# Performance work log

Hardware: AMD Instinct MI355X
Metric: run time of the kernel (lower is better)

The kernel has to match this reference:

```python
import jax, jax.numpy as jnp
import numpy as np
from jax.scipy.special import logsumexp

ITERS = 50
EPS = 0.005
B, N, D = 8, 2048, 3


def _sq_cost(x, y):
    x2 = jnp.sum(x * x, axis=-1)  # [B,N]
    y2 = jnp.sum(y * y, axis=-1)  # [B,M]
    c = x2[:, :, None] + y2[:, None, :] - 2.0 * jnp.einsum('bnd,bmd->bnm', x, y)
    return jnp.maximum(c, 0.0)


def setup_inputs() -> dict:
    key = jax.random.key(0)
    k1, k2 = jax.random.split(key)
    input1 = jax.random.normal(k1, (B, N, D), dtype=jnp.float32)
    input2 = jax.random.normal(k2, (B, N, D), dtype=jnp.float32)
    return {"input1": input1, "input2": input2}


def reference(input1, input2):
    # Approximate EMD between equal-size point sets, as in emdModule(x, y, eps, iters):
    # iterative entropic-regularized (Sinkhorn/auction-style) assignment on the
    # squared-distance cost, eps = entropic temperature, iters = sweeps.
    eps = jnp.float32(EPS)
    b, n, _ = input1.shape
    m = input2.shape[1]
    C = _sq_cost(input1, input2)  # [B,N,M]
    log_mu = -jnp.log(jnp.float32(n))
    log_nu = -jnp.log(jnp.float32(m))

    def body(carry, _):
        f, g = carry  # duals [B,N], [B,M]
        f = eps * (log_mu - logsumexp((g[:, None, :] - C) / eps, axis=2))
        g = eps * (log_nu - logsumexp((f[:, :, None] - C) / eps, axis=1))
        return (f, g), None

    f0 = jnp.zeros((b, n), dtype=C.dtype)
    g0 = jnp.zeros((b, m), dtype=C.dtype)
    (f, g), _ = jax.lax.scan(body, (f0, g0), None, length=ITERS)

    # transport plan; each row sums to 1/N (soft assignment)
    P = jnp.exp((f[:, :, None] + g[:, None, :] - C) / eps)  # [B,N,M]
    # per-point assigned squared distance (dis of emdModule), then .mean()
    dis = jnp.sum(P * C, axis=-1) * jnp.float32(n)  # [B,N]
    return jnp.mean(dis)
```

## Files before the change

kernel.cpp:

```cpp
#include <hip/hip_runtime.h>
#include <math.h>

#define NB 8
#define NN 2048
#define NM 2048
#define NITERS 50

static constexpr float F_EPS  = 0.005f;
static constexpr float LOG2E  = 1.4426950408889634f;
static constexpr float KK     = LOG2E / F_EPS;
static constexpr float TWOK   = 2.0f * KK;
static constexpr float NEG_LOG2N = -11.0f;

__device__ __forceinline__ float fexp2(float x) { return __builtin_amdgcn_exp2f(x); }
__device__ __forceinline__ float flog2(float x) { return __builtin_amdgcn_logf(x); }

__global__ void pack_init(const float* __restrict__ V, float4* __restrict__ Pout, int total)
{
    int i = blockIdx.x * blockDim.x + threadIdx.x;
    if (i < total) {
        float v0 = V[3*i], v1 = V[3*i+1], v2 = V[3*i+2];
        float s  = fmaf(v0, v0, fmaf(v1, v1, v2*v2));
        Pout[i]  = make_float4(v0, v1, v2, -KK * s);
    }
}

__global__ __launch_bounds__(256, 4) void sink_update(
    const float4* __restrict__ Pin,
    const float*  __restrict__ Vraw,
    float4*       __restrict__ Pout)
{
    __shared__ float2 part [32][65];
    __shared__ float2 part2[32][9];
    const int tid  = threadIdx.x;
    const int lane = tid & 63;
    const int wave = tid >> 6;
    const int wgs_per_b = NN / 32;
    const int b       = blockIdx.x / wgs_per_b;
    const int rowbase = (blockIdx.x % wgs_per_b) * 32;

    float xs0[8], xs1[8], xs2[8];
    {
        const float* vb = Vraw + ((size_t)(b * NN + rowbase + wave * 8)) * 3;
        #pragma unroll
        for (int r = 0; r < 8; ++r) {
            xs0[r] = TWOK * vb[r*3+0];
            xs1[r] = TWOK * vb[r*3+1];
            xs2[r] = TWOK * vb[r*3+2];
        }
    }

    const float4* __restrict__ pp = Pin + b * NM + lane;

    float rm[8], rs[8];
    #pragma unroll
    for (int r = 0; r < 8; ++r) { rm[r] = -1e30f; rs[r] = 0.f; }

    for (int ib = 0; ib < 8; ++ib) {
        const float4 p0 = pp[(ib*4 + 0) * 64];
        const float4 p1 = pp[(ib*4 + 1) * 64];
        const float4 p2 = pp[(ib*4 + 2) * 64];
        const float4 p3 = pp[(ib*4 + 3) * 64];
        #pragma unroll
        for (int r = 0; r < 8; ++r) {
            const float z0 = fmaf(xs0[r], p0.x, fmaf(xs1[r], p0.y, fmaf(xs2[r], p0.z, p0.w)));
            const float z1 = fmaf(xs0[r], p1.x, fmaf(xs1[r], p1.y, fmaf(xs2[r], p1.z, p1.w)));
            const float z2 = fmaf(xs0[r], p2.x, fmaf(xs1[r], p2.y, fmaf(xs2[r], p2.z, p2.w)));
            const float z3 = fmaf(xs0[r], p3.x, fmaf(xs1[r], p3.y, fmaf(xs2[r], p3.z, p3.w)));
            const float cm = fmaxf(fmaxf(z0, z1), fmaxf(z2, z3));
            const float nm = fmaxf(rm[r], cm);
            const float s  = (fexp2(z0 - nm) + fexp2(z1 - nm))
                           + (fexp2(z2 - nm) + fexp2(z3 - nm));
            rs[r] = fmaf(rs[r], fexp2(rm[r] - nm), s);
            rm[r] = nm;
        }
    }

    #pragma unroll
    for (int r = 0; r < 8; ++r) part[wave*8 + r][lane] = make_float2(rm[r], rs[r]);
    __syncthreads();

    {
        const int row = tid >> 3, seg = tid & 7;
        float m8 = -1e30f;
        float2 v[8];
        #pragma unroll
        for (int k = 0; k < 8; ++k) { v[k] = part[row][seg*8 + k]; m8 = fmaxf(m8, v[k].x); }
        float s8 = 0.f;
        #pragma unroll
        for (int k = 0; k < 8; ++k) s8 = fmaf(v[k].y, fexp2(v[k].x - m8), s8);
        part2[row][seg] = make_float2(m8, s8);
    }
    __syncthreads();

    if (tid < 32) {
        float gm = -1e30f;
        float2 v[8];
        #pragma unroll
        for (int k = 0; k < 8; ++k) { v[k] = part2[tid][k]; gm = fmaxf(gm, v[k].x); }
        float s = 0.f;
        #pragma unroll
        for (int k = 0; k < 8; ++k) s = fmaf(v[k].y, fexp2(v[k].x - gm), s);
        const float lse2 = gm + flog2(s);
        const int n0 = rowbase + tid;
        const float* vp = Vraw + ((size_t)(b * NN + n0)) * 3;
        Pout[b * NN + n0] = make_float4(vp[0], vp[1], vp[2], NEG_LOG2N - lse2);
    }
}

__global__ __launch_bounds__(256, 4) void final_loss(
    const float4* __restrict__ Px, const float4* __restrict__ Py,
    float* __restrict__ out)
{
    __shared__ float wsum[4];
    const int tid  = threadIdx.x;
    const int lane = tid & 63;
    const int wave = tid >> 6;
    const int wgs_per_b = NN / 32;
    const int b       = blockIdx.x / wgs_per_b;
    const int rowbase = (blockIdx.x % wgs_per_b) * 32;

    float xr0[8], xr1[8], xr2[8], Af[8], xq[8];
    {
        const float4* xb = Px + b * NN + rowbase + wave * 8;
        #pragma unroll
        for (int r = 0; r < 8; ++r) {
            const float4 xp = xb[r];
            xr0[r] = xp.x; xr1[r] = xp.y; xr2[r] = xp.z; Af[r] = xp.w;
            xq[r]  = fmaf(xp.x, xp.x, fmaf(xp.y, xp.y, xp.z * xp.z));
        }
    }

    const float4* __restrict__ pp = Py + b * NM + lane;

    float acc = 0.f;
    for (int i = 0; i < 32; ++i) {
        const float4 p = pp[i * 64];
        const float ysq = fmaf(p.x, p.x, fmaf(p.y, p.y, p.z * p.z));
        #pragma unroll
        for (int r = 0; r < 8; ++r) {
            const float dot = fmaf(xr0[r], p.x, fmaf(xr1[r], p.y, xr2[r] * p.z));
            const float cc  = fmaxf(fmaf(-2.f, dot, xq[r] + ysq), 0.f);
            const float zp  = fmaf(TWOK, dot, Af[r] + p.w);
            acc = fmaf(fexp2(zp), cc, acc);
        }
    }
    #pragma unroll
    for (int o = 32; o > 0; o >>= 1) acc += __shfl_xor(acc, o);
    if (lane == 0) wsum[wave] = acc;
    __syncthreads();
    if (tid == 0) {
        atomicAdd(out, (wsum[0] + wsum[1] + wsum[2] + wsum[3]) * (1.0f / NB));
    }
}

extern "C" void kernel_launch(void* const* d_in, const int* in_sizes, int n_in,
                              void* d_out, int out_size, void* d_ws, size_t ws_size,
                              hipStream_t stream)
{
    const float* x = (const float*)d_in[0];
    const float* y = (const float*)d_in[1];
    float4* Px = (float4*)d_ws;
    float4* Py = Px + NB * NN;

    pack_init<<<(NB * NM + 255) / 256, 256, 0, stream>>>(y, Py, NB * NM);

    for (int it = 0; it < NITERS; ++it) {
        sink_update<<<NB * NN / 32, 256, 0, stream>>>(Py, x, Px);
        sink_update<<<NB * NM / 32, 256, 0, stream>>>(Px, y, Py);
    }

    hipMemsetAsync(d_out, 0, sizeof(float), stream);
    final_loss<<<NB * NN / 32, 256, 0, stream>>>(Px, Py, (float*)d_out);
}
```

Measured before the change: 1.147 ms.

## Fuse all Sinkhorn sweeps into one persistent kernel with per-batch grid barriers

Replaces the 100 sink_update launches plus the init and final-loss kernels with a single persistent kernel of 512 workgroups. Each group of 64 workgroups, one per batch, synchronises through an atomic counter barrier with sleep-polling between half-sweeps. This removes per-launch overhead and the gaps between dependent kernels. In exchange it depends on all 512 workgroups being co-resident, since otherwise the spin barrier deadlocks, and it adds atomic polling cost at every phase.

After: 3.504 ms. +205.3%, slower.

```diff
diff --git a/kernel.cpp b/kernel.cpp
--- a/kernel.cpp
+++ b/kernel.cpp
@@ -15,33 +15,37 @@
 __device__ __forceinline__ float fexp2(float x) { return __builtin_amdgcn_exp2f(x); }
 __device__ __forceinline__ float flog2(float x) { return __builtin_amdgcn_logf(x); }
 
-__global__ void pack_init(const float* __restrict__ V, float4* __restrict__ Pout, int total)
-{
-    int i = blockIdx.x * blockDim.x + threadIdx.x;
-    if (i < total) {
-        float v0 = V[3*i], v1 = V[3*i+1], v2 = V[3*i+2];
-        float s  = fmaf(v0, v0, fmaf(v1, v1, v2*v2));
-        Pout[i]  = make_float4(v0, v1, v2, -KK * s);
-    }
-}
-
-__global__ __launch_bounds__(256, 4) void sink_update(
-    const float4* __restrict__ Pin,
-    const float*  __restrict__ Vraw,
-    float4*       __restrict__ Pout)
-{
-    __shared__ float2 part [32][65];
-    __shared__ float2 part2[32][9];
+struct SmemT {
+    float2 part [32][65];
+    float2 part2[32][9];
+    float  wsum[4];
+};
+
+__device__ __forceinline__ void batch_barrier(int* cnt, int phase)
+{
+    __syncthreads();
+    if (threadIdx.x == 0) {
+        __hip_atomic_fetch_add(cnt, 1, __ATOMIC_RELEASE, __HIP_MEMORY_SCOPE_AGENT);
+        const int target = 64 * phase;
+        while (__hip_atomic_load(cnt, __ATOMIC_ACQUIRE, __HIP_MEMORY_SCOPE_AGENT) < target)
+            __builtin_amdgcn_s_sleep(1);
+    }
+    __syncthreads();
+}
+
+__device__ __forceinline__ void half_sweep(
+    const float4* __restrict__ Pin_b,
+    const float*  __restrict__ Vrow,
+    float4*       __restrict__ Pout_row,
+    SmemT& sm)
+{
     const int tid  = threadIdx.x;
     const int lane = tid & 63;
     const int wave = tid >> 6;
-    const int wgs_per_b = NN / 32;
-    const int b       = blockIdx.x / wgs_per_b;
-    const int rowbase = (blockIdx.x % wgs_per_b) * 32;
 
     float xs0[8], xs1[8], xs2[8];
     {
-        const float* vb = Vraw + ((size_t)(b * NN + rowbase + wave * 8)) * 3;
+        const float* vb = Vrow + (size_t)(wave * 8) * 3;
         #pragma unroll
         for (int r = 0; r < 8; ++r) {
             xs0[r] = TWOK * vb[r*3+0];
@@ -50,7 +54,7 @@
         }
     }
 
-    const float4* __restrict__ pp = Pin + b * NM + lane;
+    const float4* __restrict__ pp = Pin_b + lane;
 
     float rm[8], rs[8];
     #pragma unroll
@@ -77,7 +81,7 @@
     }
 
     #pragma unroll
-    for (int r = 0; r < 8; ++r) part[wave*8 + r][lane] = make_float2(rm[r], rs[r]);
+    for (int r = 0; r < 8; ++r) sm.part[wave*8 + r][lane] = make_float2(rm[r], rs[r]);
     __syncthreads();
 
     {
@@ -85,11 +89,11 @@
         float m8 = -1e30f;
         float2 v[8];
         #pragma unroll
-        for (int k = 0; k < 8; ++k) { v[k] = part[row][seg*8 + k]; m8 = fmaxf(m8, v[k].x); }
+        for (int k = 0; k < 8; ++k) { v[k] = sm.part[row][seg*8 + k]; m8 = fmaxf(m8, v[k].x); }
         float s8 = 0.f;
         #pragma unroll
         for (int k = 0; k < 8; ++k) s8 = fmaf(v[k].y, fexp2(v[k].x - m8), s8);
-        part2[row][seg] = make_float2(m8, s8);
+        sm.part2[row][seg] = make_float2(m8, s8);
     }
     __syncthreads();
 
@@ -97,60 +101,86 @@
         float gm = -1e30f;
         float2 v[8];
         #pragma unroll
-        for (int k = 0; k < 8; ++k) { v[k] = part2[tid][k]; gm = fmaxf(gm, v[k].x); }
+        for (int k = 0; k < 8; ++k) { v[k] = sm.part2[tid][k]; gm = fmaxf(gm, v[k].x); }
         float s = 0.f;
         #pragma unroll
         for (int k = 0; k < 8; ++k) s = fmaf(v[k].y, fexp2(v[k].x - gm), s);
         const float lse2 = gm + flog2(s);
-        const int n0 = rowbase + tid;
-        const float* vp = Vraw + ((size_t)(b * NN + n0)) * 3;
-        Pout[b * NN + n0] = make_float4(vp[0], vp[1], vp[2], NEG_LOG2N - lse2);
-    }
-}
-
-__global__ __launch_bounds__(256, 4) void final_loss(
-    const float4* __restrict__ Px, const float4* __restrict__ Py,
-    float* __restrict__ out)
-{
-    __shared__ float wsum[4];
-    const int tid  = threadIdx.x;
-    const int lane = tid & 63;
-    const int wave = tid >> 6;
-    const int wgs_per_b = NN / 32;
-    const int b       = blockIdx.x / wgs_per_b;
-    const int rowbase = (blockIdx.x % wgs_per_b) * 32;
-
-    float xr0[8], xr1[8], xr2[8], Af[8], xq[8];
+        const float* vp = Vrow + (size_t)tid * 3;
+        Pout_row[tid] = make_float4(vp[0], vp[1], vp[2], NEG_LOG2N - lse2);
+    }
+    __syncthreads();
+}
+
+__global__ __launch_bounds__(256, 2) void sinkhorn_persist(
+    const float* __restrict__ X, const float* __restrict__ Y,
+    float4* __restrict__ Px, float4* __restrict__ Py,
+    int* __restrict__ cnt, float* __restrict__ out)
+{
+    __shared__ SmemT sm;
+    const int tid     = threadIdx.x;
+    const int b       = blockIdx.x & 7;
+    const int rowbase = (blockIdx.x >> 3) * 32;
+    int* mycnt = cnt + b * 16;
+
+    const float*  Xrow = X + ((size_t)(b * NN + rowbase)) * 3;
+    const float*  Yrow = Y + ((size_t)(b * NM + rowbase)) * 3;
+    float4* PxRow = Px + b * NN + rowbase;
+    float4* PyRow = Py + b * NM + rowbase;
+    const float4* PxB = Px + b * NN;
+    const float4* PyB = Py + b * NM;
+
+    if (tid < 32) {
+        const float* vp = Yrow + (size_t)tid * 3;
+        const float v0 = vp[0], v1 = vp[1], v2 = vp[2];
+        const float sq = fmaf(v0, v0, fmaf(v1, v1, v2*v2));
+        PyRow[tid] = make_float4(v0, v1, v2, -KK * sq);
+    }
+
+    int phase = 1;
+    batch_barrier(mycnt, phase);
+
+    #pragma unroll 1
+    for (int it = 0; it < NITERS; ++it) {
+        half_sweep(PyB, Xrow, PxRow, sm);
+        batch_barrier(mycnt, ++phase);
+        half_sweep(PxB, Yrow, PyRow, sm);
+        batch_barrier(mycnt, ++phase);
+    }
+
     {
-        const float4* xb = Px + b * NN + rowbase + wave * 8;
+        const int lane = tid & 63;
+        const int wave = tid >> 6;
+
+        float xr0[8], xr1[8], xr2[8], Af[8], xq[8];
+        const float4* xb = PxRow + wave * 8;
         #pragma unroll
         for (int r = 0; r < 8; ++r) {
             const float4 xp = xb[r];
             xr0[r] = xp.x; xr1[r] = xp.y; xr2[r] = xp.z; Af[r] = xp.w;
             xq[r]  = fmaf(xp.x, xp.x, fmaf(xp.y, xp.y, xp.z * xp.z));
         }
-    }
-
-    const float4* __restrict__ pp = Py + b * NM + lane;
-
-    float acc = 0.f;
-    for (int i = 0; i < 32; ++i) {
-        const float4 p = pp[i * 64];
-        const float ysq = fmaf(p.x, p.x, fmaf(p.y, p.y, p.z * p.z));
-        #pragma unroll
-        for (int r = 0; r < 8; ++r) {
-            const float dot = fmaf(xr0[r], p.x, fmaf(xr1[r], p.y, xr2[r] * p.z));
-            const float cc  = fmaxf(fmaf(-2.f, dot, xq[r] + ysq), 0.f);
-            const float zp  = fmaf(TWOK, dot, Af[r] + p.w);
-            acc = fmaf(fexp2(zp), cc, acc);
-        }
-    }
-    #pragma unroll
-    for (int o = 32; o > 0; o >>= 1) acc += __shfl_xor(acc, o);
-    if (lane == 0) wsum[wave] = acc;
-    __syncthreads();
-    if (tid == 0) {
-        atomicAdd(out, (wsum[0] + wsum[1] + wsum[2] + wsum[3]) * (1.0f / NB));
+
+        const float4* __restrict__ pp = PyB + lane;
+        float acc = 0.f;
+        for (int i = 0; i < 32; ++i) {
+            const float4 p = pp[i * 64];
+            const float ysq = fmaf(p.x, p.x, fmaf(p.y, p.y, p.z * p.z));
+            #pragma unroll
+            for (int r = 0; r < 8; ++r) {
+                const float dot = fmaf(xr0[r], p.x, fmaf(xr1[r], p.y, xr2[r] * p.z));
+                const float cc  = fmaxf(fmaf(-2.f, dot, xq[r] + ysq), 0.f);
+                const float zp  = fmaf(TWOK, dot, Af[r] + p.w);
+                acc = fmaf(fexp2(zp), cc, acc);
+            }
+        }
+        #pragma unroll
+        for (int o = 32; o > 0; o >>= 1) acc += __shfl_xor(acc, o);
+        if (lane == 0) sm.wsum[wave] = acc;
+        __syncthreads();
+        if (tid == 0) {
+            atomicAdd(out, (sm.wsum[0] + sm.wsum[1] + sm.wsum[2] + sm.wsum[3]) * (1.0f / NB));
+        }
     }
 }
 
@@ -162,14 +192,10 @@
     const float* y = (const float*)d_in[1];
     float4* Px = (float4*)d_ws;
     float4* Py = Px + NB * NN;
-
-    pack_init<<<(NB * NM + 255) / 256, 256, 0, stream>>>(y, Py, NB * NM);
-
-    for (int it = 0; it < NITERS; ++it) {
-        sink_update<<<NB * NN / 32, 256, 0, stream>>>(Py, x, Px);
-        sink_update<<<NB * NM / 32, 256, 0, stream>>>(Px, y, Py);
-    }
-
+    int*    cnt = (int*)((char*)d_ws + (size_t)(NB * NN + NB * NM) * sizeof(float4));
+
+    hipMemsetAsync(cnt, 0, NB * 16 * sizeof(int), stream);
     hipMemsetAsync(d_out, 0, sizeof(float), stream);
-    final_loss<<<NB * NN / 32, 256, 0, stream>>>(Px, Py, (float*)d_out);
-}
+
+    sinkhorn_persist<<<NB * NN / 32, 256, 0, stream>>>(x, y, Px, Py, cnt, (float*)d_out);
+}
```

## Split column range across waves and double-buffer column loads

Applied to the files above, without the earlier changes.

Each workgroup now covers 16 rows instead of 32. Its four waves are arranged as 2 row-groups by 2 column halves, so each wave scans 1024 columns instead of all 2048. This doubles the grid to 1024 blocks for better occupancy across the CUs. The column-point loads are software-prefetched one batch ahead so global latency overlaps the exp/FMA work. In exchange the shared-memory reduction becomes wider (16 partials per row), and each column point is read by twice as many workgroups.

Result: faster. 1.120 ms (-2.4%).

```diff
diff --git a/kernel.cpp b/kernel.cpp
--- a/kernel.cpp
+++ b/kernel.cpp
@@ -30,18 +30,20 @@
     const float*  __restrict__ Vraw,
     float4*       __restrict__ Pout)
 {
-    __shared__ float2 part [32][65];
-    __shared__ float2 part2[32][9];
+    __shared__ float2 part [16][129];
+    __shared__ float2 part2[16][17];
     const int tid  = threadIdx.x;
     const int lane = tid & 63;
     const int wave = tid >> 6;
-    const int wgs_per_b = NN / 32;
+    const int rw   = wave & 1;
+    const int mh   = wave >> 1;
+    const int wgs_per_b = NN / 16;
     const int b       = blockIdx.x / wgs_per_b;
-    const int rowbase = (blockIdx.x % wgs_per_b) * 32;
+    const int rowbase = (blockIdx.x % wgs_per_b) * 16;
 
     float xs0[8], xs1[8], xs2[8];
     {
-        const float* vb = Vraw + ((size_t)(b * NN + rowbase + wave * 8)) * 3;
+        const float* vb = Vraw + ((size_t)(b * NN + rowbase + rw * 8)) * 3;
         #pragma unroll
         for (int r = 0; r < 8; ++r) {
             xs0[r] = TWOK * vb[r*3+0];
@@ -50,23 +52,29 @@
         }
     }
 
-    const float4* __restrict__ pp = Pin + b * NM + lane;
+    const float4* __restrict__ pp = Pin + b * NM + mh * 1024 + lane;
 
     float rm[8], rs[8];
     #pragma unroll
     for (int r = 0; r < 8; ++r) { rm[r] = -1e30f; rs[r] = 0.f; }
 
-    for (int ib = 0; ib < 8; ++ib) {
-        const float4 p0 = pp[(ib*4 + 0) * 64];
-        const float4 p1 = pp[(ib*4 + 1) * 64];
-        const float4 p2 = pp[(ib*4 + 2) * 64];
-        const float4 p3 = pp[(ib*4 + 3) * 64];
+    float4 c0 = pp[0*64], c1 = pp[1*64], c2 = pp[2*64], c3 = pp[3*64];
+
+    #pragma unroll
+    for (int ib = 0; ib < 4; ++ib) {
+        float4 n0, n1, n2, n3;
+        if (ib < 3) {
+            n0 = pp[(ib*4 + 4) * 64];
+            n1 = pp[(ib*4 + 5) * 64];
+            n2 = pp[(ib*4 + 6) * 64];
+            n3 = pp[(ib*4 + 7) * 64];
+        }
         #pragma unroll
         for (int r = 0; r < 8; ++r) {
-            const float z0 = fmaf(xs0[r], p0.x, fmaf(xs1[r], p0.y, fmaf(xs2[r], p0.z, p0.w)));
-            const float z1 = fmaf(xs0[r], p1.x, fmaf(xs1[r], p1.y, fmaf(xs2[r], p1.z, p1.w)));
-            const float z2 = fmaf(xs0[r], p2.x, fmaf(xs1[r], p2.y, fmaf(xs2[r], p2.z, p2.w)));
-            const float z3 = fmaf(xs0[r], p3.x, fmaf(xs1[r], p3.y, fmaf(xs2[r], p3.z, p3.w)));
+            const float z0 = fmaf(xs0[r], c0.x, fmaf(xs1[r], c0.y, fmaf(xs2[r], c0.z, c0.w)));
+            const float z1 = fmaf(xs0[r], c1.x, fmaf(xs1[r], c1.y, fmaf(xs2[r], c1.z, c1.w)));
+            const float z2 = fmaf(xs0[r], c2.x, fmaf(xs1[r], c2.y, fmaf(xs2[r], c2.z, c2.w)));
+            const float z3 = fmaf(xs0[r], c3.x, fmaf(xs1[r], c3.y, fmaf(xs2[r], c3.z, c3.w)));
             const float cm = fmaxf(fmaxf(z0, z1), fmaxf(z2, z3));
             const float nm = fmaxf(rm[r], cm);
             const float s  = (fexp2(z0 - nm) + fexp2(z1 - nm))
@@ -74,14 +82,16 @@
             rs[r] = fmaf(rs[r], fexp2(rm[r] - nm), s);
             rm[r] = nm;
         }
+        if (ib < 3) { c0 = n0; c1 = n1; c2 = n2; c3 = n3; }
     }
 
     #pragma unroll
-    for (int r = 0; r < 8; ++r) part[wave*8 + r][lane] = make_float2(rm[r], rs[r]);
+    for (int r = 0; r < 8; ++r)
+        part[rw*8 + r][mh*64 + lane] = make_float2(rm[r], rs[r]);
     __syncthreads();
 
     {
-        const int row = tid >> 3, seg = tid & 7;
+        const int row = tid & 15, seg = tid >> 4;
         float m8 = -1e30f;
         float2 v[8];
         #pragma unroll
@@ -93,14 +103,14 @@
     }
     __syncthreads();
 
-    if (tid < 32) {
+    if (tid < 16) {
         float gm = -1e30f;
-        float2 v[8];
+        float2 v[16];
         #pragma unroll
-        for (int k = 0; k < 8; ++k) { v[k] = part2[tid][k]; gm = fmaxf(gm, v[k].x); }
+        for (int k = 0; k < 16; ++k) { v[k] = part2[tid][k]; gm = fmaxf(gm, v[k].x); }
         float s = 0.f;
         #pragma unroll
-        for (int k = 0; k < 8; ++k) s = fmaf(v[k].y, fexp2(v[k].x - gm), s);
+        for (int k = 0; k < 16; ++k) s = fmaf(v[k].y, fexp2(v[k].x - gm), s);
         const float lse2 = gm + flog2(s);
         const int n0 = rowbase + tid;
         const float* vp = Vraw + ((size_t)(b * NN + n0)) * 3;
@@ -116,13 +126,15 @@
     const int tid  = threadIdx.x;
     const int lane = tid & 63;
     const int wave = tid >> 6;
-    const int wgs_per_b = NN / 32;
+    const int rw   = wave & 1;
+    const int mh   = wave >> 1;
+    const int wgs_per_b = NN / 16;
     const int b       = blockIdx.x / wgs_per_b;
-    const int rowbase = (blockIdx.x % wgs_per_b) * 32;
+    const int rowbase = (blockIdx.x % wgs_per_b) * 16;
 
     float xr0[8], xr1[8], xr2[8], Af[8], xq[8];
     {
-        const float4* xb = Px + b * NN + rowbase + wave * 8;
+        const float4* xb = Px + b * NN + rowbase + rw * 8;
         #pragma unroll
         for (int r = 0; r < 8; ++r) {
             const float4 xp = xb[r];
@@ -131,19 +143,23 @@
         }
     }
 
-    const float4* __restrict__ pp = Py + b * NM + lane;
+    const float4* __restrict__ pp = Py + b * NM + mh * 1024 + lane;
 
     float acc = 0.f;
-    for (int i = 0; i < 32; ++i) {
-        const float4 p = pp[i * 64];
-        const float ysq = fmaf(p.x, p.x, fmaf(p.y, p.y, p.z * p.z));
+    float4 cur = pp[0];
+    #pragma unroll
+    for (int i = 0; i < 16; ++i) {
+        float4 nxt;
+        if (i < 15) nxt = pp[(i + 1) * 64];
+        const float ysq = fmaf(cur.x, cur.x, fmaf(cur.y, cur.y, cur.z * cur.z));
         #pragma unroll
         for (int r = 0; r < 8; ++r) {
-            const float dot = fmaf(xr0[r], p.x, fmaf(xr1[r], p.y, xr2[r] * p.z));
+            const float dot = fmaf(xr0[r], cur.x, fmaf(xr1[r], cur.y, xr2[r] * cur.z));
             const float cc  = fmaxf(fmaf(-2.f, dot, xq[r] + ysq), 0.f);
-            const float zp  = fmaf(TWOK, dot, Af[r] + p.w);
+            const float zp  = fmaf(TWOK, dot, Af[r] + cur.w);
             acc = fmaf(fexp2(zp), cc, acc);
         }
+        if (i < 15) cur = nxt;
     }
     #pragma unroll
     for (int o = 32; o > 0; o >>= 1) acc += __shfl_xor(acc, o);
@@ -166,10 +182,10 @@
     pack_init<<<(NB * NM + 255) / 256, 256, 0, stream>>>(y, Py, NB * NM);
 
     for (int it = 0; it < NITERS; ++it) {
-        sink_update<<<NB * NN / 32, 256, 0, stream>>>(Py, x, Px);
-        sink_update<<<NB * NM / 32, 256, 0, stream>>>(Px, y, Py);
+        sink_update<<<NB * NN / 16, 256, 0, stream>>>(Py, x, Px);
+        sink_update<<<NB * NM / 16, 256, 0, stream>>>(Px, y, Py);
     }
 
     hipMemsetAsync(d_out, 0, sizeof(float), stream);
-    final_loss<<<NB * NN / 32, 256, 0, stream>>>(Px, Py, (float*)d_out);
+    final_loss<<<NB * NN / 16, 256, 0, stream>>>(Px, Py, (float*)d_out);
 }
```

## Fuse all Sinkhorn sweeps into one persistent kernel with dataflow flags

Applied to the files above, without the earlier changes.

Replaces the 100 per-half-iteration kernel launches plus init and final kernels with a single persistent kernel of 1024 workgroups. Each workgroup owns 16 rows per batch and publishes its dual updates via agent-scope atomic stores and per-group progress flags. Consumers spin-wait on those flags group by group, prefetching the next group, which removes launch overhead and global barriers between sweeps. It relies on all workgroups being co-resident (1024 WGs at 4 per CU on 256 CUs) or it can deadlock, and it adds spin-polling and uncached loads.

Result: slower. 2.815 ms (+145.4%).

```diff
diff --git a/kernel.cpp b/kernel.cpp
--- a/kernel.cpp
+++ b/kernel.cpp
@@ -6,151 +6,188 @@
 #define NM 2048
 #define NITERS 50
 
-static constexpr float F_EPS  = 0.005f;
 static constexpr float LOG2E  = 1.4426950408889634f;
-static constexpr float KK     = LOG2E / F_EPS;
+static constexpr float KK     = LOG2E / 0.005f;
 static constexpr float TWOK   = 2.0f * KK;
 static constexpr float NEG_LOG2N = -11.0f;
 
 __device__ __forceinline__ float fexp2(float x) { return __builtin_amdgcn_exp2f(x); }
 __device__ __forceinline__ float flog2(float x) { return __builtin_amdgcn_logf(x); }
 
-__global__ void pack_init(const float* __restrict__ V, float4* __restrict__ Pout, int total)
-{
-    int i = blockIdx.x * blockDim.x + threadIdx.x;
-    if (i < total) {
-        float v0 = V[3*i], v1 = V[3*i+1], v2 = V[3*i+2];
-        float s  = fmaf(v0, v0, fmaf(v1, v1, v2*v2));
-        Pout[i]  = make_float4(v0, v1, v2, -KK * s);
-    }
-}
-
-__global__ __launch_bounds__(256, 4) void sink_update(
-    const float4* __restrict__ Pin,
-    const float*  __restrict__ Vraw,
-    float4*       __restrict__ Pout)
-{
-    __shared__ float2 part [32][65];
-    __shared__ float2 part2[32][9];
-    const int tid  = threadIdx.x;
-    const int lane = tid & 63;
-    const int wave = tid >> 6;
-    const int wgs_per_b = NN / 32;
-    const int b       = blockIdx.x / wgs_per_b;
-    const int rowbase = (blockIdx.x % wgs_per_b) * 32;
-
-    float xs0[8], xs1[8], xs2[8];
-    {
-        const float* vb = Vraw + ((size_t)(b * NN + rowbase + wave * 8)) * 3;
+__device__ __forceinline__ float ld_sc1(const float* p) {
+    return __hip_atomic_load(p, __ATOMIC_RELAXED, __HIP_MEMORY_SCOPE_AGENT);
+}
+__device__ __forceinline__ void st_sc1(float* p, float v) {
+    __hip_atomic_store(p, v, __ATOMIC_RELAXED, __HIP_MEMORY_SCOPE_AGENT);
+}
+__device__ __forceinline__ int ld_flag(const int* p) {
+    return __hip_atomic_load(p, __ATOMIC_RELAXED, __HIP_MEMORY_SCOPE_AGENT);
+}
+__device__ __forceinline__ void st_flag(int* p, int v) {
+    __hip_atomic_store(p, v, __ATOMIC_RELAXED, __HIP_MEMORY_SCOPE_AGENT);
+}
+
+__device__ __forceinline__ void wait_group(const int* __restrict__ fl, int g,
+                                           int target, int lane)
+{
+    const int* p = fl + g * 8 + (lane & 7);
+    for (;;) {
+        const int v = ld_flag(p);
+        if (__all(v >= target)) break;
+        __builtin_amdgcn_s_sleep(2);
+    }
+}
+
+__device__ __forceinline__ float sweep_lse(
+    const float*  __restrict__ Din,
+    const float4* __restrict__ Qin,
+    const int*    __restrict__ fl,
+    int target, float xs0, float xs1, float xs2, int ms, int lane)
+{
+    float rm = -1e30f, rs = 0.f;
+    float d[8], dn[8];
+
+    wait_group(fl, 0, target, lane);
+    wait_group(fl, 1, target, lane);
+    #pragma unroll
+    for (int j = 0; j < 8; ++j) d[j]  = ld_sc1(Din + 0 * 128 + j * 16 + ms);
+    #pragma unroll
+    for (int j = 0; j < 8; ++j) dn[j] = ld_sc1(Din + 1 * 128 + j * 16 + ms);
+    int pv = ld_flag(fl + 2 * 8 + (lane & 7));
+
+    #pragma unroll 1
+    for (int g = 0; g < 16; ++g) {
+        const float4* __restrict__ qb = Qin + g * 128 + ms;
         #pragma unroll
-        for (int r = 0; r < 8; ++r) {
-            xs0[r] = TWOK * vb[r*3+0];
-            xs1[r] = TWOK * vb[r*3+1];
-            xs2[r] = TWOK * vb[r*3+2];
-        }
-    }
-
-    const float4* __restrict__ pp = Pin + b * NM + lane;
-
-    float rm[8], rs[8];
-    #pragma unroll
-    for (int r = 0; r < 8; ++r) { rm[r] = -1e30f; rs[r] = 0.f; }
-
-    for (int ib = 0; ib < 8; ++ib) {
-        const float4 p0 = pp[(ib*4 + 0) * 64];
-        const float4 p1 = pp[(ib*4 + 1) * 64];
-        const float4 p2 = pp[(ib*4 + 2) * 64];
-        const float4 p3 = pp[(ib*4 + 3) * 64];
-        #pragma unroll
-        for (int r = 0; r < 8; ++r) {
-            const float z0 = fmaf(xs0[r], p0.x, fmaf(xs1[r], p0.y, fmaf(xs2[r], p0.z, p0.w)));
-            const float z1 = fmaf(xs0[r], p1.x, fmaf(xs1[r], p1.y, fmaf(xs2[r], p1.z, p1.w)));
-            const float z2 = fmaf(xs0[r], p2.x, fmaf(xs1[r], p2.y, fmaf(xs2[r], p2.z, p2.w)));
-            const float z3 = fmaf(xs0[r], p3.x, fmaf(xs1[r], p3.y, fmaf(xs2[r], p3.z, p3.w)));
+        for (int c = 0; c < 2; ++c) {
+            const float4 q0 = qb[(4 * c + 0) * 16];
+            const float4 q1 = qb[(4 * c + 1) * 16];
+            const float4 q2 = qb[(4 * c + 2) * 16];
+            const float4 q3 = qb[(4 * c + 3) * 16];
+            const float z0 = d[4*c+0] + fmaf(xs0, q0.x, fmaf(xs1, q0.y, fmaf(xs2, q0.z, q0.w)));
+            const float z1 = d[4*c+1] + fmaf(xs0, q1.x, fmaf(xs1, q1.y, fmaf(xs2, q1.z, q1.w)));
+            const float z2 = d[4*c+2] + fmaf(xs0, q2.x, fmaf(xs1, q2.y, fmaf(xs2, q2.z, q2.w)));
+            const float z3 = d[4*c+3] + fmaf(xs0, q3.x, fmaf(xs1, q3.y, fmaf(xs2, q3.z, q3.w)));
             const float cm = fmaxf(fmaxf(z0, z1), fmaxf(z2, z3));
-            const float nm = fmaxf(rm[r], cm);
+            const float nm = fmaxf(rm, cm);
             const float s  = (fexp2(z0 - nm) + fexp2(z1 - nm))
                            + (fexp2(z2 - nm) + fexp2(z3 - nm));
-            rs[r] = fmaf(rs[r], fexp2(rm[r] - nm), s);
-            rm[r] = nm;
+            rs = fmaf(rs, fexp2(rm - nm), s);
+            rm = nm;
         }
+        if (g < 14) {
+            if (!__all(pv >= target)) wait_group(fl, g + 2, target, lane);
+            #pragma unroll
+            for (int j = 0; j < 8; ++j) d[j] = dn[j];
+            #pragma unroll
+            for (int j = 0; j < 8; ++j) dn[j] = ld_sc1(Din + (g + 2) * 128 + j * 16 + ms);
+            if (g < 13) pv = ld_flag(fl + (g + 3) * 8 + (lane & 7));
+        } else if (g == 14) {
+            #pragma unroll
+            for (int j = 0; j < 8; ++j) d[j] = dn[j];
+        }
     }
 
     #pragma unroll
-    for (int r = 0; r < 8; ++r) part[wave*8 + r][lane] = make_float2(rm[r], rs[r]);
-    __syncthreads();
-
-    {
-        const int row = tid >> 3, seg = tid & 7;
-        float m8 = -1e30f;
-        float2 v[8];
-        #pragma unroll
-        for (int k = 0; k < 8; ++k) { v[k] = part[row][seg*8 + k]; m8 = fmaxf(m8, v[k].x); }
-        float s8 = 0.f;
-        #pragma unroll
-        for (int k = 0; k < 8; ++k) s8 = fmaf(v[k].y, fexp2(v[k].x - m8), s8);
-        part2[row][seg] = make_float2(m8, s8);
-    }
-    __syncthreads();
-
-    if (tid < 32) {
-        float gm = -1e30f;
-        float2 v[8];
-        #pragma unroll
-        for (int k = 0; k < 8; ++k) { v[k] = part2[tid][k]; gm = fmaxf(gm, v[k].x); }
-        float s = 0.f;
-        #pragma unroll
-        for (int k = 0; k < 8; ++k) s = fmaf(v[k].y, fexp2(v[k].x - gm), s);
-        const float lse2 = gm + flog2(s);
-        const int n0 = rowbase + tid;
-        const float* vp = Vraw + ((size_t)(b * NN + n0)) * 3;
-        Pout[b * NN + n0] = make_float4(vp[0], vp[1], vp[2], NEG_LOG2N - lse2);
-    }
-}
-
-__global__ __launch_bounds__(256, 4) void final_loss(
-    const float4* __restrict__ Px, const float4* __restrict__ Py,
+    for (int w = 1; w <= 8; w <<= 1) {
+        const float om = __shfl_xor(rm, w);
+        const float os = __shfl_xor(rs, w);
+        const float nm = fmaxf(rm, om);
+        rs = fmaf(rs, fexp2(rm - nm), os * fexp2(om - nm));
+        rm = nm;
+    }
+    return rm + flog2(rs);
+}
+
+__global__ __launch_bounds__(256, 4) void sinkhorn_df(
+    const float* __restrict__ X, const float* __restrict__ Y,
+    float4* __restrict__ Qx, float4* __restrict__ Qy,
+    float* __restrict__ Dx, float* __restrict__ Dy,
+    int* __restrict__ Fx, int* __restrict__ Fy,
     float* __restrict__ out)
 {
     __shared__ float wsum[4];
     const int tid  = threadIdx.x;
     const int lane = tid & 63;
-    const int wave = tid >> 6;
-    const int wgs_per_b = NN / 32;
-    const int b       = blockIdx.x / wgs_per_b;
-    const int rowbase = (blockIdx.x % wgs_per_b) * 32;
-
-    float xr0[8], xr1[8], xr2[8], Af[8], xq[8];
+    const int ms   = tid & 15;
+    const int row  = tid >> 4;
+    const int b    = blockIdx.x & 7;
+    const int wgb  = blockIdx.x >> 3;
+    const int myrow = wgb * 16 + row;
+
+    const float* xp = X + (size_t)(b * NN + myrow) * 3;
+    const float* yp = Y + (size_t)(b * NM + myrow) * 3;
+    const float x0 = xp[0], x1 = xp[1], x2 = xp[2];
+    const float y0 = yp[0], y1 = yp[1], y2 = yp[2];
+    const float xsq = fmaf(x0, x0, fmaf(x1, x1, x2 * x2));
+    const float ysq = fmaf(y0, y0, fmaf(y1, y1, y2 * y2));
+    const float qxw = -KK * xsq, qyw = -KK * ysq;
+    const float xs0 = TWOK * x0, xs1 = TWOK * x1, xs2 = TWOK * x2;
+    const float ys0 = TWOK * y0, ys1 = TWOK * y1, ys2 = TWOK * y2;
+
+    float4* QxB = Qx + b * NN;  float4* QyB = Qy + b * NM;
+    float*  DxB = Dx + b * NN;  float*  DyB = Dy + b * NM;
+    int* fxB = Fx + b * 128;    int* fyB = Fy + b * 128;
+
+    if (ms == 0) {
+        float4* q = QxB + myrow;
+        st_sc1(&q->x, x0); st_sc1(&q->y, x1); st_sc1(&q->z, x2); st_sc1(&q->w, qxw);
+    } else if (ms == 1) {
+        float4* q = QyB + myrow;
+        st_sc1(&q->x, y0); st_sc1(&q->y, y1); st_sc1(&q->z, y2); st_sc1(&q->w, qyw);
+    } else if (ms == 2) {
+        st_sc1(DyB + myrow, 0.f);
+    }
+    asm volatile("s_waitcnt vmcnt(0)" ::: "memory");
+    __syncthreads();
+    if (tid == 0) { st_flag(fxB + wgb, 1); st_flag(fyB + wgb, 1); }
+
+    float Af = 0.f;
+
+    #pragma unroll 1
+    for (int it = 0; it < NITERS; ++it) {
+        float lse2 = sweep_lse(DyB, QyB, fyB, it + 1, xs0, xs1, xs2, ms, lane);
+        const float fd = NEG_LOG2N - lse2 - qxw;
+        Af = NEG_LOG2N - lse2;
+        if (ms == 0) st_sc1(DxB + myrow, fd);
+        asm volatile("s_waitcnt vmcnt(0)" ::: "memory");
+        __syncthreads();
+        if (tid == 0) st_flag(fxB + wgb, it + 2);
+
+        lse2 = sweep_lse(DxB, QxB, fxB, it + 2, ys0, ys1, ys2, ms, lane);
+        const float gd = NEG_LOG2N - lse2 - qyw;
+        if (ms == 0) st_sc1(DyB + myrow, gd);
+        asm volatile("s_waitcnt vmcnt(0)" ::: "memory");
+        __syncthreads();
+        if (tid == 0) st_flag(fyB + wgb, it + 2);
+    }
+
     {
-        const float4* xb = Px + b * NN + rowbase + wave * 8;
+        const int target = NITERS + 1;
+        float acc = 0.f;
+        #pragma unroll 1
+        for (int g = 0; g < 16; ++g) {
+            wait_group(fyB, g, target, lane);
+            const float4* __restrict__ qb = QyB + g * 128 + ms;
+            const float*  __restrict__ db = DyB + g * 128 + ms;
+            #pragma unroll
+            for (int j = 0; j < 8; ++j) {
+                const float4 q  = qb[j * 16];
+                const float  dg = ld_sc1(db + j * 16);
+                const float chain = fmaf(xs0, q.x, fmaf(xs1, q.y, fmaf(xs2, q.z, q.w)));
+                const float zp  = Af + dg + chain;
+                const float dot = fmaf(x0, q.x, fmaf(x1, q.y, x2 * q.z));
+                const float yq  = fmaf(q.x, q.x, fmaf(q.y, q.y, q.z * q.z));
+                const float cc  = fmaxf(fmaf(-2.f, dot, xsq + yq), 0.f);
+                acc = fmaf(fexp2(zp), cc, acc);
+            }
+        }
         #pragma unroll
-        for (int r = 0; r < 8; ++r) {
-            const float4 xp = xb[r];
-            xr0[r] = xp.x; xr1[r] = xp.y; xr2[r] = xp.z; Af[r] = xp.w;
-            xq[r]  = fmaf(xp.x, xp.x, fmaf(xp.y, xp.y, xp.z * xp.z));
-        }
-    }
-
-    const float4* __restrict__ pp = Py + b * NM + lane;
-
-    float acc = 0.f;
-    for (int i = 0; i < 32; ++i) {
-        const float4 p = pp[i * 64];
-        const float ysq = fmaf(p.x, p.x, fmaf(p.y, p.y, p.z * p.z));
-        #pragma unroll
-        for (int r = 0; r < 8; ++r) {
-            const float dot = fmaf(xr0[r], p.x, fmaf(xr1[r], p.y, xr2[r] * p.z));
-            const float cc  = fmaxf(fmaf(-2.f, dot, xq[r] + ysq), 0.f);
-            const float zp  = fmaf(TWOK, dot, Af[r] + p.w);
-            acc = fmaf(fexp2(zp), cc, acc);
-        }
-    }
-    #pragma unroll
-    for (int o = 32; o > 0; o >>= 1) acc += __shfl_xor(acc, o);
-    if (lane == 0) wsum[wave] = acc;
-    __syncthreads();
-    if (tid == 0) {
-        atomicAdd(out, (wsum[0] + wsum[1] + wsum[2] + wsum[3]) * (1.0f / NB));
+        for (int w = 1; w <= 32; w <<= 1) acc += __shfl_xor(acc, w);
+        if (lane == 0) wsum[tid >> 6] = acc;
+        __syncthreads();
+        if (tid == 0)
+            atomicAdd(out, (wsum[0] + wsum[1] + wsum[2] + wsum[3]) * (1.0f / NB));
     }
 }
 
@@ -160,16 +197,16 @@
 {
     const float* x = (const float*)d_in[0];
     const float* y = (const float*)d_in[1];
-    float4* Px = (float4*)d_ws;
-    float4* Py = Px + NB * NN;
-
-    pack_init<<<(NB * NM + 255) / 256, 256, 0, stream>>>(y, Py, NB * NM);
-
-    for (int it = 0; it < NITERS; ++it) {
-        sink_update<<<NB * NN / 32, 256, 0, stream>>>(Py, x, Px);
-        sink_update<<<NB * NM / 32, 256, 0, stream>>>(Px, y, Py);
-    }
-
+    float4* Qx = (float4*)d_ws;
+    float4* Qy = Qx + NB * NN;
+    float*  Dx = (float*)(Qy + NB * NM);
+    float*  Dy = Dx + NB * NN;
+    int*    Fx = (int*)(Dy + NB * NM);
+    int*    Fy = Fx + NB * 128;
+
+    hipMemsetAsync(Fx, 0, 2 * NB * 128 * sizeof(int), stream);
     hipMemsetAsync(d_out, 0, sizeof(float), stream);
-    final_loss<<<NB * NN / 32, 256, 0, stream>>>(Px, Py, (float*)d_out);
-}
+
+    sinkhorn_df<<<NB * NN / 16, 256, 0, stream>>>(x, y, Qx, Qy, Dx, Dy, Fx, Fy,
+                                                  (float*)d_out);
+}
```
